# Performance work log

Measured on AMD Instinct MI355X. Metric: run time of the kernel, lower is better.

Reference implementation:

```python
import jax, jax.numpy as jnp
import numpy as np

K = 3  # kernel_size per dim
DIM = 3
NUM_K = K ** DIM  # 27
# the 2^3 corner offsets of the linear B-spline support
OFFS = np.array([[(s >> d) & 1 for d in range(DIM)] for s in range(2 ** DIM)], dtype=np.int32)  # [8,3]
STRIDES = np.array([K ** d for d in range(DIM)], dtype=np.int32)  # [1,3,9]


def bspline_basis(pseudo):
    """Open B-spline basis, degree 1. pseudo: [E,3] in [0,1]. Returns basis [E,8], kidx [E,8]."""
    v = pseudo * (K - 1)
    i0 = jnp.clip(jnp.floor(v), 0, K - 2)
    f = v - i0  # fractional part in [0,1]
    i0 = i0.astype(jnp.int32)
    offs = jnp.asarray(OFFS)  # [8,3]
    w = jnp.where(offs[None].astype(bool), f[:, None, :], 1.0 - f[:, None, :])  # [E,8,3]
    basis = jnp.prod(w, axis=-1)  # [E,8]
    kidx = jnp.sum((i0[:, None, :] + offs[None]) * jnp.asarray(STRIDES)[None, None, :], axis=-1)  # [E,8]
    return basis, kidx


def spline_conv(x, src, dst, pseudo, W, Wroot, b, num_nodes):
    """SplineConv (degree 1, mean aggregation, root weight + bias)."""
    cout = W.shape[-1]
    xW = jnp.einsum('nc,kco->nko', x, W)  # [N,27,Cout]
    basis, kidx = bspline_basis(pseudo)
    flat = src[:, None] * NUM_K + kidx  # [E,8]
    g = xW.reshape(-1, cout)[flat]  # [E,8,Cout] -- dominant gather
    msg = jnp.einsum('es,eso->eo', basis, g)  # [E,Cout]
    agg = jax.ops.segment_sum(msg, dst, num_segments=num_nodes)
    cnt = jax.ops.segment_sum(jnp.ones((src.shape[0],), x.dtype), dst, num_segments=num_nodes)
    return agg / jnp.maximum(cnt, 1.0)[:, None] + x @ Wroot + b


def seg_max(x, seg, num_segments):
    m = jax.ops.segment_max(x, seg, num_segments=num_segments)
    return jnp.where(jnp.isfinite(m), m, 0.0)  # empty clusters -> 0


def setup_inputs() -> dict:
    key = jax.random.key(0)
    ks = jax.random.split(key, 16)
    N, E, B = 80000, 1280000, 16
    N1, N2 = N // 2, N1 if False else (N // 2) // 2  # N1=40000, N2=20000
    N1 = N // 2
    N2 = N1 // 2
    x = jax.random.normal(ks[0], (N, 2), dtype=jnp.float32)
    edge_index = jax.random.randint(ks[1], (2, E), 0, N, dtype=jnp.int32)
    edge_attr = jax.random.uniform(ks[2], (E, 3), dtype=jnp.float32)
    batch = jnp.sort(jax.random.randint(ks[3], (N,), 0, B, dtype=jnp.int32))
    cluster1 = jax.random.randint(ks[4], (N,), 0, N1, dtype=jnp.int32)
    cluster2 = jax.random.randint(ks[5], (N1,), 0, N2, dtype=jnp.int32)
    W1 = jax.random.normal(ks[6], (NUM_K, 2, 8), dtype=jnp.float32) * 0.3
    root1 = jax.random.normal(ks[7], (2, 8), dtype=jnp.float32) * 0.3
    b1 = jnp.zeros((8,), jnp.float32)
    W2 = jax.random.normal(ks[8], (NUM_K, 8, 16), dtype=jnp.float32) * 0.2
    root2 = jax.random.normal(ks[9], (8, 16), dtype=jnp.float32) * 0.2
    b2 = jnp.zeros((16,), jnp.float32)
    fc1_w = jax.random.normal(ks[10], (16, 64), dtype=jnp.float32) * 0.2
    fc1_b = jnp.zeros((64,), jnp.float32)
    fc2_w = jax.random.normal(ks[11], (64, 1), dtype=jnp.float32) * 0.2
    fc2_b = jnp.zeros((1,), jnp.float32)
    return dict(x=x, edge_index=edge_index, edge_attr=edge_attr, batch=batch,
                cluster1=cluster1, cluster2=cluster2,
                W1=W1, root1=root1, b1=b1, W2=W2, root2=root2, b2=b2,
                fc1_w=fc1_w, fc1_b=fc1_b, fc2_w=fc2_w, fc2_b=fc2_b)


def reference(x, edge_index, edge_attr, batch, cluster1, cluster2,
              W1, root1, b1, W2, root2, b2, fc1_w, fc1_b, fc2_w, fc2_b):
    N = x.shape[0]
    N1 = cluster1.max() * 0 + cluster2.shape[0]  # static: 40000
    N1 = cluster2.shape[0]
    N2 = N1 // 2
    B = 16
    src, dst = edge_index[0], edge_index[1]
    # level 1: SplineConv + ELU
    h = jax.nn.elu(spline_conv(x, src, dst, edge_attr, W1, root1, b1, N))
    # max_pool with precomputed cluster assignment (replaces graclus)
    x1 = seg_max(h, cluster1, N1)
    batch1 = jnp.maximum(jax.ops.segment_max(batch, cluster1, num_segments=N1), 0)
    src2 = cluster1[src]
    dst2 = cluster1[dst]
    # level 2: SplineConv + ELU on coarsened graph
    h2 = jax.nn.elu(spline_conv(x1, src2, dst2, edge_attr, W2, root2, b2, N1))
    x2 = seg_max(h2, cluster2, N2)
    batch2 = jnp.maximum(jax.ops.segment_max(batch1, cluster2, num_segments=N2), 0)
    # scatter_mean over graphs
    s = jax.ops.segment_sum(x2, batch2, num_segments=B)
    c = jax.ops.segment_sum(jnp.ones((N2,), x.dtype), batch2, num_segments=B)
    g = s / jnp.maximum(c, 1.0)[:, None]  # [B,16]
    g = jax.nn.elu(g @ fc1_w + fc1_b)  # dropout is identity in eval mode
    return jax.nn.elu(g @ fc2_w + fc2_b)  # [B,1]
```

## Files before the change

kernel.cpp:

```cpp
#include <hip/hip_runtime.h>
#include <hip/hip_fp16.h>
#include <math.h>


__device__ __forceinline__ float eluf(float x) {
    return x > 0.f ? x : (expf(x) - 1.f);
}

__device__ __forceinline__ float hlo(int v) {
    __half2 h; *(int*)&h = v; return __low2float(h);
}
__device__ __forceinline__ float hhi(int v) {
    __half2 h; *(int*)&h = v; return __high2float(h);
}

typedef _Float16 half2v __attribute__((ext_vector_type(2)));

__device__ __forceinline__ half2v uash2(unsigned u) {
    half2v h; *(unsigned*)&h = u; return h;
}

__device__ __forceinline__ float dot2f(half2v a, half2v b, float c) {
#if __has_builtin(__builtin_amdgcn_fdot2)
    return __builtin_amdgcn_fdot2(a, b, c, false);
#else
    return c + (float)a[0] * (float)b[0] + (float)a[1] * (float)b[1];
#endif
}

#define W1_STRIDE 20
#define W2H_STRIDE 68


__global__ __launch_bounds__(256) void hist_kernel(
    const int* __restrict__ ei, const int* __restrict__ cluster1,
    const int* __restrict__ cluster2,
    int* __restrict__ deg, int* __restrict__ rank,
    int* __restrict__ cdeg, int* __restrict__ rankC,
    int* __restrict__ c2deg, int* __restrict__ rank2,
    int E, int N, int N1)
{
    int i = blockIdx.x * 256 + threadIdx.x;
    if (i < E)  rank[i]  = atomicAdd(&deg[ei[E + i]], 1);
    if (i < N)  rankC[i] = atomicAdd(&cdeg[cluster1[i]], 1);
    if (i < N1) rank2[i] = atomicAdd(&c2deg[cluster2[i]], 1);
}

#define SCAN_CHUNK 4096

__global__ __launch_bounds__(256) void scan_a(
    const int* __restrict__ in0, int* __restrict__ out0, int* __restrict__ aux0, int L0, int nb0,
    const int* __restrict__ in1, int* __restrict__ out1, int* __restrict__ aux1, int L1, int nb1,
    const int* __restrict__ in2, int* __restrict__ out2, int* __restrict__ aux2, int L2)
{
    int b = blockIdx.x;
    const int* in; int* out; int* aux; int L;
    if (b < nb0)            { in = in0; out = out0; aux = aux0; L = L0; }
    else if (b < nb0 + nb1) { b -= nb0; in = in1; out = out1; aux = aux1; L = L1; }
    else                    { b -= nb0 + nb1; in = in2; out = out2; aux = aux2; L = L2; }

    __shared__ int ls[256];
    int t = threadIdx.x;
    int base = b * SCAN_CHUNK + t * 16;
    int v[16];
    int s = 0;
#pragma unroll
    for (int j = 0; j < 16; ++j) {
        int val = (base + j < L) ? in[base + j] : 0;
        v[j] = s;
        s += val;
    }
    ls[t] = s;
    __syncthreads();
    for (int off = 1; off < 256; off <<= 1) {
        int tv = (t >= off) ? ls[t - off] : 0;
        __syncthreads();
        ls[t] += tv;
        __syncthreads();
    }
    int excl = ls[t] - s;
#pragma unroll
    for (int j = 0; j < 16; ++j)
        if (base + j < L) out[base + j] = excl + v[j];
    if (t == 255) aux[b] = ls[255];
}

__global__ __launch_bounds__(64) void scan_b(
    int* __restrict__ aux0, int nb0, int* __restrict__ off0, int L0,
    int* __restrict__ aux1, int nb1, int* __restrict__ off1, int L1,
    int* __restrict__ aux2, int nb2, int* __restrict__ off2, int L2)
{
    if (threadIdx.x != 0) return;
    int* aux; int nb; int* off; int L;
    if (blockIdx.x == 0)      { aux = aux0; nb = nb0; off = off0; L = L0; }
    else if (blockIdx.x == 1) { aux = aux1; nb = nb1; off = off1; L = L1; }
    else                      { aux = aux2; nb = nb2; off = off2; L = L2; }
    int run = 0;
    for (int j = 0; j < nb; ++j) { int tv = aux[j]; aux[j] = run; run += tv; }
    off[L] = run;
}

__global__ __launch_bounds__(256) void scan_c(
    int* __restrict__ out0, const int* __restrict__ aux0, int L0, int nb0,
    int* __restrict__ out1, const int* __restrict__ aux1, int L1, int nb1,
    int* __restrict__ out2, const int* __restrict__ aux2, int L2)
{
    int b = blockIdx.x;
    int* out; const int* aux; int L;
    if (b < nb0)            { out = out0; aux = aux0; L = L0; }
    else if (b < nb0 + nb1) { b -= nb0; out = out1; aux = aux1; L = L1; }
    else                    { b -= nb0 + nb1; out = out2; aux = aux2; L = L2; }
    int add = aux[b];
    int base = b * SCAN_CHUNK + threadIdx.x * 16;
#pragma unroll
    for (int j = 0; j < 16; ++j)
        if (base + j < L) out[base + j] += add;
}

__global__ __launch_bounds__(256) void scatB_kernel(
    const int* __restrict__ ei, const float* __restrict__ attr,
    const int* __restrict__ cluster1, const int* __restrict__ cluster2,
    const float2* __restrict__ x, const float* __restrict__ W1,
    const int* __restrict__ doffs, const int* __restrict__ rank,
    const int* __restrict__ coff, const int* __restrict__ rankC,
    const int* __restrict__ c2off, const int* __restrict__ rank2,
    int* __restrict__ nidx, int* __restrict__ n1idx,
    int4* __restrict__ rec4, int E, int N, int N1)
{
    __shared__ float lw[27 * W1_STRIDE];
    for (int i = threadIdx.x; i < 27 * 16; i += 256)
        lw[(i >> 4) * W1_STRIDE + (i & 15)] = W1[i];
    __syncthreads();

    int i = blockIdx.x * 256 + threadIdx.x;
    if (i < E) {
        int s = ei[i], d = ei[E + i];
        int p = doffs[d] + rank[i];

        float vx = attr[3 * i] * 2.f, vy = attr[3 * i + 1] * 2.f, vz = attr[3 * i + 2] * 2.f;
        float ix = fmaxf(fminf(floorf(vx), 1.f), 0.f);
        float iy = fmaxf(fminf(floorf(vy), 1.f), 0.f);
        float iz = fmaxf(fminf(floorf(vz), 1.f), 0.f);
        float fx = vx - ix, fy = vy - iy, fz = vz - iz;
        int ibase = (int)ix + 3 * (int)iy + 9 * (int)iz;

        float2 xv = x[s];
        float wxv[2] = {1.f - fx, fx}, wyv[2] = {1.f - fy, fy}, wzv[2] = {1.f - fz, fz};
        float m[8];
#pragma unroll
        for (int o = 0; o < 8; ++o) m[o] = 0.f;
#pragma unroll
        for (int j = 0; j < 8; ++j) {
            int cx = j & 1, cy = (j >> 1) & 1, cz = j >> 2;
            float w = wxv[cx] * wyv[cy] * wzv[cz];
            const float* Wk = &lw[(ibase + cx + 3 * cy + 9 * cz) * W1_STRIDE];
            float a = w * xv.x, bb = w * xv.y;
            const float4 wa0 = *(const float4*)&Wk[0];
            const float4 wa1 = *(const float4*)&Wk[4];
            const float4 wb0 = *(const float4*)&Wk[8];
            const float4 wb1 = *(const float4*)&Wk[12];
            m[0] += a * wa0.x + bb * wb0.x;
            m[1] += a * wa0.y + bb * wb0.y;
            m[2] += a * wa0.z + bb * wb0.z;
            m[3] += a * wa0.w + bb * wb0.w;
            m[4] += a * wa1.x + bb * wb1.x;
            m[5] += a * wa1.y + bb * wb1.y;
            m[6] += a * wa1.z + bb * wb1.z;
            m[7] += a * wa1.w + bb * wb1.w;
        }

        unsigned hfx = __half_as_ushort(__float2half_rn(fx));
        unsigned hfy = __half_as_ushort(__float2half_rn(fy));
        unsigned hfz = __half_as_ushort(__float2half_rn(fz));
        int s2 = cluster1[s];
        int4 ra = make_int4(s2 | (ibase << 16),
                            (int)(hfx | (hfy << 16)), (int)hfz, 0);
        __half2 h01 = __floats2half2_rn(m[0], m[1]);
        __half2 h23 = __floats2half2_rn(m[2], m[3]);
        __half2 h45 = __floats2half2_rn(m[4], m[5]);
        __half2 h67 = __floats2half2_rn(m[6], m[7]);
        int4 rb = make_int4(*(int*)&h01, *(int*)&h23, *(int*)&h45, *(int*)&h67);
        rec4[2 * (size_t)p]     = ra;
        rec4[2 * (size_t)p + 1] = rb;
    }
    if (i < N)  nidx[coff[cluster1[i]] + rankC[i]] = i;
    if (i < N1) n1idx[c2off[cluster2[i]] + rank2[i]] = i;
}

__global__ __launch_bounds__(256) void reduce1_kernel(
    const int* __restrict__ doffs, const unsigned short* __restrict__ recU,
    float* __restrict__ M1, int N)
{
    int t = blockIdx.x * 256 + threadIdx.x;
    if (t >= N * 8) return;
    int d = t >> 3, ch = t & 7;
    int beg = doffs[d], end = doffs[d + 1];
    float acc = 0.f;
    for (int p = beg; p < end; ++p)
        acc += __half2float(__ushort_as_half(recU[(size_t)p * 16 + 8 + ch]));
    M1[t] = acc / fmaxf((float)(end - beg), 1.f);
}

__global__ __launch_bounds__(256) void node1_kernel(
    const int* __restrict__ coff, const int* __restrict__ nidx,
    const float* __restrict__ M1, const float2* __restrict__ x,
    const float* __restrict__ root1, const float* __restrict__ b1,
    const int* __restrict__ batch,
    float* __restrict__ x1c, unsigned short* __restrict__ x1chU,
    int* __restrict__ batch1, int N1)
{
    int t = blockIdx.x * 256 + threadIdx.x;
    if (t >= N1 * 8) return;
    int c = t >> 3, ch = t & 7;
    int cb = coff[c], ce = coff[c + 1];
    float r0 = root1[ch], r1 = root1[8 + ch], bo = b1[ch];
    float hm = -INFINITY;
    int bm = 0;
    for (int idx = cb; idx < ce; ++idx) {
        int d = nidx[idx];
        float2 xv = x[d];
        float h = eluf(M1[d * 8 + ch] + xv.x * r0 + xv.y * r1 + bo);
        hm = fmaxf(hm, h);
        bm = max(bm, batch[d]);
    }
    if (ce == cb) hm = 0.f;
    x1c[t] = hm;
    x1chU[t] = __half_as_ushort(__float2half_rn(hm));
    if (ch == 0) batch1[c] = bm;
}

__global__ __launch_bounds__(256) void edge2m_kernel(
    const int4* __restrict__ rec4, const unsigned short* __restrict__ x1chU,
    const float* __restrict__ W2, unsigned short* __restrict__ msg2h, int E)
{
    __shared__ unsigned lwh[27 * W2H_STRIDE];
    for (int i = threadIdx.x; i < 27 * 64; i += 256) {
        int k = i >> 6, r = i & 63;
        int o = r >> 2, c2 = r & 3;
        float a = W2[(k * 8 + 2 * c2) * 16 + o];
        float b = W2[(k * 8 + 2 * c2 + 1) * 16 + o];
        __half2 h = __floats2half2_rn(a, b);
        lwh[k * W2H_STRIDE + r] = *(unsigned*)&h;
    }
    __syncthreads();

    int t = blockIdx.x * 256 + threadIdx.x;
    if (t >= E * 4) return;
    int p = t >> 2, oq = t & 3;
    int4 m = rec4[2 * (size_t)p];
    int s2 = m.x & 0xFFFF;
    int ibase = (m.x >> 16) & 31;
    float fx = hlo(m.y), fy = hhi(m.y), fz = hlo(m.z);

    const uint4 xv4 = *(const uint4*)&x1chU[(size_t)s2 * 8];
    half2v xh0 = uash2(xv4.x), xh1 = uash2(xv4.y),
           xh2 = uash2(xv4.z), xh3 = uash2(xv4.w);

    float wx0 = 1.f - fx, wy0 = 1.f - fy, wz0 = 1.f - fz;
    float acc0 = 0.f, acc1 = 0.f, acc2 = 0.f, acc3 = 0.f;
#pragma unroll
    for (int j = 0; j < 8; ++j) {
        int cx = j & 1, cy = (j >> 1) & 1, cz = j >> 2;
        float w = (cx ? fx : wx0) * (cy ? fy : wy0) * (cz ? fz : wz0);
        int k = ibase + cx + 3 * cy + 9 * cz;
        const unsigned* base = &lwh[k * W2H_STRIDE + oq * 16];
        uint4 v0 = *(const uint4*)(base);
        uint4 v1 = *(const uint4*)(base + 4);
        uint4 v2 = *(const uint4*)(base + 8);
        uint4 v3 = *(const uint4*)(base + 12);
        float s0 = dot2f(xh0, uash2(v0.x), dot2f(xh1, uash2(v0.y),
                   dot2f(xh2, uash2(v0.z), dot2f(xh3, uash2(v0.w), 0.f))));
        float s1 = dot2f(xh0, uash2(v1.x), dot2f(xh1, uash2(v1.y),
                   dot2f(xh2, uash2(v1.z), dot2f(xh3, uash2(v1.w), 0.f))));
        float s2v = dot2f(xh0, uash2(v2.x), dot2f(xh1, uash2(v2.y),
                    dot2f(xh2, uash2(v2.z), dot2f(xh3, uash2(v2.w), 0.f))));
        float s3 = dot2f(xh0, uash2(v3.x), dot2f(xh1, uash2(v3.y),
                   dot2f(xh2, uash2(v3.z), dot2f(xh3, uash2(v3.w), 0.f))));
        acc0 = fmaf(w, s0, acc0);
        acc1 = fmaf(w, s1, acc1);
        acc2 = fmaf(w, s2v, acc2);
        acc3 = fmaf(w, s3, acc3);
    }
    __half2 lo = __floats2half2_rn(acc0, acc1);
    __half2 hi = __floats2half2_rn(acc2, acc3);
    uint2 outv = make_uint2(*(unsigned*)&lo, *(unsigned*)&hi);
    *(uint2*)&msg2h[(size_t)p * 16 + oq * 4] = outv;
}

__global__ __launch_bounds__(256) void reduce2_kernel(
    const int* __restrict__ coff, const int* __restrict__ nidx,
    const int* __restrict__ doffs, const unsigned short* __restrict__ msg2h,
    float* __restrict__ M2, int N1)
{
    int t = blockIdx.x * 256 + threadIdx.x;
    if (t >= N1 * 16) return;
    int c = t >> 4, o = t & 15;
    float acc = 0.f;
    int cnt = 0;
    int cb = coff[c], ce = coff[c + 1];
    for (int idx = cb; idx < ce; ++idx) {
        int d = nidx[idx];
        int beg = doffs[d], end = doffs[d + 1];
        cnt += end - beg;
        for (int p = beg; p < end; ++p)
            acc += __half2float(__ushort_as_half(msg2h[(size_t)p * 16 + o]));
    }
    M2[t] = acc / fmaxf((float)cnt, 1.f);
}

__global__ __launch_bounds__(256) void node2_kernel(
    const int* __restrict__ c2off, const int* __restrict__ n1idx,
    const float* __restrict__ M2, const float* __restrict__ x1c,
    const float* __restrict__ root2, const float* __restrict__ b2,
    const int* __restrict__ batch1,
    float* __restrict__ gsum, float* __restrict__ gcnt, int N2)
{
    __shared__ float ls[16 * 16];
    __shared__ float lc[16];
    for (int i = threadIdx.x; i < 256; i += 256) ls[i] = 0.f;
    if (threadIdx.x < 16) lc[threadIdx.x] = 0.f;
    __syncthreads();

    int c2 = blockIdx.x * 256 + threadIdx.x;
    if (c2 < N2) {
        int cb = c2off[c2], ce = c2off[c2 + 1];
        float hm[16];
#pragma unroll
        for (int o = 0; o < 16; ++o) hm[o] = -INFINITY;
        int bm = 0;
        for (int idx = cb; idx < ce; ++idx) {
            int n1 = n1idx[idx];
            const float4* xr4 = (const float4*)&x1c[(size_t)n1 * 8];
            float4 xa = xr4[0], xb = xr4[1];
            float xr[8] = {xa.x, xa.y, xa.z, xa.w, xb.x, xb.y, xb.z, xb.w};
#pragma unroll
            for (int o = 0; o < 16; ++o) {
                float v = M2[(size_t)n1 * 16 + o] + b2[o];
#pragma unroll
                for (int c8 = 0; c8 < 8; ++c8) v += xr[c8] * root2[c8 * 16 + o];
                hm[o] = fmaxf(hm[o], eluf(v));
            }
            bm = max(bm, batch1[n1]);
        }
        if (ce == cb) {
#pragma unroll
            for (int o = 0; o < 16; ++o) hm[o] = 0.f;
        }
#pragma unroll
        for (int o = 0; o < 16; ++o) atomicAdd(&ls[bm * 16 + o], hm[o]);
        atomicAdd(&lc[bm], 1.f);
    }
    __syncthreads();
    for (int i = threadIdx.x; i < 256; i += 256) unsafeAtomicAdd(&gsum[i], ls[i]);
    if (threadIdx.x < 16) unsafeAtomicAdd(&gcnt[threadIdx.x], lc[threadIdx.x]);
}

__global__ __launch_bounds__(256) void head_kernel(
    const float* __restrict__ gsum, const float* __restrict__ gcnt,
    const float* __restrict__ fc1_w, const float* __restrict__ fc1_b,
    const float* __restrict__ fc2_w, const float* __restrict__ fc2_b,
    float* __restrict__ out, int B)
{
    __shared__ float g[16 * 16];
    __shared__ float h1[16 * 64];
    int t = threadIdx.x;
    if (t < B * 16) {
        int b = t >> 4;
        g[t] = gsum[t] / fmaxf(gcnt[b], 1.f);
    }
    __syncthreads();
    for (int j = t; j < B * 64; j += 256) {
        int b = j >> 6, jj = j & 63;
        float s = fc1_b[jj];
#pragma unroll
        for (int c = 0; c < 16; ++c) s += g[b * 16 + c] * fc1_w[c * 64 + jj];
        h1[j] = eluf(s);
    }
    __syncthreads();
    if (t < B) {
        float s = fc2_b[0];
#pragma unroll
        for (int j = 0; j < 64; ++j) s += h1[t * 64 + j] * fc2_w[j];
        out[t] = eluf(s);
    }
}

extern "C" void kernel_launch(void* const* d_in, const int* in_sizes, int n_in,
                              void* d_out, int out_size, void* d_ws, size_t ws_size,
                              hipStream_t stream)
{
    const float* x        = (const float*)d_in[0];
    const int*   ei       = (const int*)  d_in[1];
    const float* attr     = (const float*)d_in[2];
    const int*   batch    = (const int*)  d_in[3];
    const int*   cluster1 = (const int*)  d_in[4];
    const int*   cluster2 = (const int*)  d_in[5];
    const float* W1       = (const float*)d_in[6];
    const float* root1    = (const float*)d_in[7];
    const float* b1       = (const float*)d_in[8];
    const float* W2       = (const float*)d_in[9];
    const float* root2    = (const float*)d_in[10];
    const float* b2       = (const float*)d_in[11];
    const float* fc1_w    = (const float*)d_in[12];
    const float* fc1_b    = (const float*)d_in[13];
    const float* fc2_w    = (const float*)d_in[14];
    const float* fc2_b    = (const float*)d_in[15];

    const int N  = in_sizes[0] / 2;
    const int E  = in_sizes[1] / 2;
    const int N1 = in_sizes[5];
    const int N2 = N1 / 2;
    const int B  = out_size;

    const int nb0 = (N  + SCAN_CHUNK - 1) / SCAN_CHUNK;
    const int nb1 = (N1 + SCAN_CHUNK - 1) / SCAN_CHUNK;
    const int nb2 = (N2 + SCAN_CHUNK - 1) / SCAN_CHUNK;

    int* wi = (int*)d_ws;
    size_t off = 0;
    auto alloc = [&](size_t n, size_t align = 1) {
        off = (off + align - 1) & ~(align - 1);
        size_t r = off; off += n; return r;
    };
    int*   deg    = wi + alloc(N);
    int*   cdeg   = wi + alloc(N1);
    int*   c2deg  = wi + alloc(N2);
    float* gsum   = (float*)(wi + alloc((size_t)B * 16));
    float* gcnt   = (float*)(wi + alloc(B));
    const size_t zcount = off;
    int*   doffs  = wi + alloc(N + 1);
    int*   coff   = wi + alloc(N1 + 1);
    int*   c2off  = wi + alloc(N2 + 1);
    int*   auxA   = wi + alloc(nb0);
    int*   auxB   = wi + alloc(nb1);
    int*   auxC   = wi + alloc(nb2);
    int*   rank   = wi + alloc(E);
    int*   rankC  = wi + alloc(N);
    int*   rank2  = wi + alloc(N1);
    int*   nidx   = wi + alloc(N);
    int*   n1idx  = wi + alloc(N1);
    int4*  rec4   = (int4*)(wi + alloc((size_t)E * 8, 8));
    unsigned short* msg2h = (unsigned short*)(wi + alloc((size_t)E * 8, 4));
    float* M1     = (float*)(wi + alloc((size_t)N * 8, 4));
    float* x1c    = (float*)(wi + alloc((size_t)N1 * 8, 4));
    unsigned short* x1chU = (unsigned short*)(wi + alloc((size_t)N1 * 4, 4));
    int*   batch1 = wi + alloc(N1);
    float* M2     = (float*)(wi + alloc((size_t)N1 * 16, 4));
    (void)ws_size;

    hipMemsetAsync(d_ws, 0, zcount * sizeof(int), stream);

    const int eb = (E + 255) / 256;
    hist_kernel<<<eb, 256, 0, stream>>>(ei, cluster1, cluster2,
                                        deg, rank, cdeg, rankC, c2deg, rank2, E, N, N1);
    scan_a<<<nb0 + nb1 + nb2, 256, 0, stream>>>(deg, doffs, auxA, N, nb0,
                                                cdeg, coff, auxB, N1, nb1,
                                                c2deg, c2off, auxC, N2);
    scan_b<<<3, 64, 0, stream>>>(auxA, nb0, doffs, N,
                                 auxB, nb1, coff, N1,
                                 auxC, nb2, c2off, N2);
    scan_c<<<nb0 + nb1 + nb2, 256, 0, stream>>>(doffs, auxA, N, nb0,
                                                coff, auxB, N1, nb1,
                                                c2off, auxC, N2);
    scatB_kernel<<<eb, 256, 0, stream>>>(ei, attr, cluster1, cluster2,
                                         (const float2*)x, W1,
                                         doffs, rank, coff, rankC, c2off, rank2,
                                         nidx, n1idx, rec4, E, N, N1);
    reduce1_kernel<<<(N * 8 + 255) / 256, 256, 0, stream>>>(
        doffs, (const unsigned short*)rec4, M1, N);
    node1_kernel<<<(N1 * 8 + 255) / 256, 256, 0, stream>>>(
        coff, nidx, M1, (const float2*)x, root1, b1, batch,
        x1c, x1chU, batch1, N1);
    edge2m_kernel<<<(E * 4 + 255) / 256, 256, 0, stream>>>(
        rec4, x1chU, W2, msg2h, E);
    reduce2_kernel<<<(N1 * 16 + 255) / 256, 256, 0, stream>>>(
        coff, nidx, doffs, msg2h, M2, N1);
    node2_kernel<<<(N2 + 255) / 256, 256, 0, stream>>>(
        c2off, n1idx, M2, x1c, root2, b2, batch1, gsum, gcnt, N2);
    head_kernel<<<1, 256, 0, stream>>>(gsum, gcnt, fc1_w, fc1_b, fc2_w, fc2_b,
                                       (float*)d_out, B);
}
```

Baseline: 358.0 us.

## Fuse level-2 edge messages and reduction via per-cluster basis accumulation

Replaces the per-edge message kernel and the separate reduction kernel with a single per-destination-cluster kernel. Each cluster first accumulates basis-weighted input features into a 27x8 shared-memory tile, then applies W2 once per kernel slot, which avoids writing and re-reading a per-edge fp16 message buffer and cuts the weight multiplies. The cost is a large shared-memory footprint (about 28KB per block), which limits occupancy. Load balance also depends on how many edges each cluster owns, and the half-precision conversion now happens on accumulated sums.

```diff
diff --git a/kernel.cpp b/kernel.cpp
--- a/kernel.cpp
+++ b/kernel.cpp
@@ -18,6 +18,11 @@
 
 __device__ __forceinline__ half2v uash2(unsigned u) {
     half2v h; *(unsigned*)&h = u; return h;
+}
+
+__device__ __forceinline__ half2v f2h2(float a, float b) {
+    __half2 h = __floats2half2_rn(a, b);
+    return *(half2v*)&h;
 }
 
 __device__ __forceinline__ float dot2f(half2v a, half2v b, float c) {
@@ -206,8 +211,7 @@
     const float* __restrict__ M1, const float2* __restrict__ x,
     const float* __restrict__ root1, const float* __restrict__ b1,
     const int* __restrict__ batch,
-    float* __restrict__ x1c, unsigned short* __restrict__ x1chU,
-    int* __restrict__ batch1, int N1)
+    float* __restrict__ x1c, int* __restrict__ batch1, int N1)
 {
     int t = blockIdx.x * 256 + threadIdx.x;
     if (t >= N1 * 8) return;
@@ -225,15 +229,19 @@
     }
     if (ce == cb) hm = 0.f;
     x1c[t] = hm;
-    x1chU[t] = __half_as_ushort(__float2half_rn(hm));
     if (ch == 0) batch1[c] = bm;
 }
 
-__global__ __launch_bounds__(256) void edge2m_kernel(
-    const int4* __restrict__ rec4, const unsigned short* __restrict__ x1chU,
-    const float* __restrict__ W2, unsigned short* __restrict__ msg2h, int E)
-{
+__global__ __launch_bounds__(256) void edge2f_kernel(
+    const int* __restrict__ coff, const int* __restrict__ nidx,
+    const int* __restrict__ doffs, const int4* __restrict__ rec4,
+    const float* __restrict__ x1c, const float* __restrict__ W2,
+    float* __restrict__ M2, int N1)
+{
+    __shared__ float A[27 * 32 * 8];
     __shared__ unsigned lwh[27 * W2H_STRIDE];
+    __shared__ float lcnt[32];
+
     for (int i = threadIdx.x; i < 27 * 64; i += 256) {
         int k = i >> 6, r = i & 63;
         int o = r >> 2, c2 = r & 3;
@@ -242,70 +250,66 @@
         __half2 h = __floats2half2_rn(a, b);
         lwh[k * W2H_STRIDE + r] = *(unsigned*)&h;
     }
-    __syncthreads();
-
-    int t = blockIdx.x * 256 + threadIdx.x;
-    if (t >= E * 4) return;
-    int p = t >> 2, oq = t & 3;
-    int4 m = rec4[2 * (size_t)p];
-    int s2 = m.x & 0xFFFF;
-    int ibase = (m.x >> 16) & 31;
-    float fx = hlo(m.y), fy = hhi(m.y), fz = hlo(m.z);
-
-    const uint4 xv4 = *(const uint4*)&x1chU[(size_t)s2 * 8];
-    half2v xh0 = uash2(xv4.x), xh1 = uash2(xv4.y),
-           xh2 = uash2(xv4.z), xh3 = uash2(xv4.w);
-
-    float wx0 = 1.f - fx, wy0 = 1.f - fy, wz0 = 1.f - fz;
-    float acc0 = 0.f, acc1 = 0.f, acc2 = 0.f, acc3 = 0.f;
-#pragma unroll
-    for (int j = 0; j < 8; ++j) {
-        int cx = j & 1, cy = (j >> 1) & 1, cz = j >> 2;
-        float w = (cx ? fx : wx0) * (cy ? fy : wy0) * (cz ? fz : wz0);
-        int k = ibase + cx + 3 * cy + 9 * cz;
-        const unsigned* base = &lwh[k * W2H_STRIDE + oq * 16];
-        uint4 v0 = *(const uint4*)(base);
-        uint4 v1 = *(const uint4*)(base + 4);
-        uint4 v2 = *(const uint4*)(base + 8);
-        uint4 v3 = *(const uint4*)(base + 12);
-        float s0 = dot2f(xh0, uash2(v0.x), dot2f(xh1, uash2(v0.y),
-                   dot2f(xh2, uash2(v0.z), dot2f(xh3, uash2(v0.w), 0.f))));
-        float s1 = dot2f(xh0, uash2(v1.x), dot2f(xh1, uash2(v1.y),
-                   dot2f(xh2, uash2(v1.z), dot2f(xh3, uash2(v1.w), 0.f))));
-        float s2v = dot2f(xh0, uash2(v2.x), dot2f(xh1, uash2(v2.y),
-                    dot2f(xh2, uash2(v2.z), dot2f(xh3, uash2(v2.w), 0.f))));
-        float s3 = dot2f(xh0, uash2(v3.x), dot2f(xh1, uash2(v3.y),
-                   dot2f(xh2, uash2(v3.z), dot2f(xh3, uash2(v3.w), 0.f))));
-        acc0 = fmaf(w, s0, acc0);
-        acc1 = fmaf(w, s1, acc1);
-        acc2 = fmaf(w, s2v, acc2);
-        acc3 = fmaf(w, s3, acc3);
-    }
-    __half2 lo = __floats2half2_rn(acc0, acc1);
-    __half2 hi = __floats2half2_rn(acc2, acc3);
-    uint2 outv = make_uint2(*(unsigned*)&lo, *(unsigned*)&hi);
-    *(uint2*)&msg2h[(size_t)p * 16 + oq * 4] = outv;
-}
-
-__global__ __launch_bounds__(256) void reduce2_kernel(
-    const int* __restrict__ coff, const int* __restrict__ nidx,
-    const int* __restrict__ doffs, const unsigned short* __restrict__ msg2h,
-    float* __restrict__ M2, int N1)
-{
-    int t = blockIdx.x * 256 + threadIdx.x;
-    if (t >= N1 * 16) return;
-    int c = t >> 4, o = t & 15;
-    float acc = 0.f;
-    int cnt = 0;
-    int cb = coff[c], ce = coff[c + 1];
-    for (int idx = cb; idx < ce; ++idx) {
-        int d = nidx[idx];
-        int beg = doffs[d], end = doffs[d + 1];
-        cnt += end - beg;
-        for (int p = beg; p < end; ++p)
-            acc += __half2float(__ushort_as_half(msg2h[(size_t)p * 16 + o]));
-    }
-    M2[t] = acc / fmaxf((float)cnt, 1.f);
+    for (int i = threadIdx.x; i < 27 * 32 * 8; i += 256) A[i] = 0.f;
+    if (threadIdx.x < 32) lcnt[threadIdx.x] = 0.f;
+    __syncthreads();
+
+    int cl = threadIdx.x >> 3, ch = threadIdx.x & 7;
+    int c = blockIdx.x * 32 + cl;
+    if (c < N1) {
+        int cnt = 0;
+        int cb = coff[c], ce = coff[c + 1];
+        for (int idx = cb; idx < ce; ++idx) {
+            int d = nidx[idx];
+            int beg = doffs[d], end = doffs[d + 1];
+            cnt += end - beg;
+            for (int p = beg; p < end; ++p) {
+                int4 m = rec4[2 * (size_t)p];
+                int s2 = m.x & 0xFFFF;
+                int ibase = (m.x >> 16) & 31;
+                float fx = hlo(m.y), fy = hhi(m.y), fz = hlo(m.z);
+                float xv = x1c[s2 * 8 + ch];
+                float wx0 = 1.f - fx, wy0 = 1.f - fy, wz0 = 1.f - fz;
+                float w00 = wy0 * wz0, w10 = fy * wz0;
+                float w01 = wy0 * fz,  w11 = fy * fz;
+                int base = ibase * 256 + cl * 8 + ch;
+                A[base]            += (wx0 * w00) * xv;
+                A[base + 1 * 256]  += (fx  * w00) * xv;
+                A[base + 3 * 256]  += (wx0 * w10) * xv;
+                A[base + 4 * 256]  += (fx  * w10) * xv;
+                A[base + 9 * 256]  += (wx0 * w01) * xv;
+                A[base + 10 * 256] += (fx  * w01) * xv;
+                A[base + 12 * 256] += (wx0 * w11) * xv;
+                A[base + 13 * 256] += (fx  * w11) * xv;
+            }
+        }
+        if (ch == 0) lcnt[cl] = (float)cnt;
+    }
+    __syncthreads();
+
+    if (c < N1) {
+        int o2 = ch;
+        float acc0 = 0.f, acc1 = 0.f;
+        for (int k = 0; k < 27; ++k) {
+            const float4* ar = (const float4*)&A[k * 256 + cl * 8];
+            float4 a0 = ar[0], a1 = ar[1];
+            half2v pa0 = f2h2(a0.x, a0.y), pa1 = f2h2(a0.z, a0.w);
+            half2v pa2 = f2h2(a1.x, a1.y), pa3 = f2h2(a1.z, a1.w);
+            const uint4 w0 = *(const uint4*)&lwh[k * W2H_STRIDE + o2 * 4];
+            const uint4 w1 = *(const uint4*)&lwh[k * W2H_STRIDE + (o2 + 8) * 4];
+            acc0 = dot2f(pa0, uash2(w0.x), acc0);
+            acc0 = dot2f(pa1, uash2(w0.y), acc0);
+            acc0 = dot2f(pa2, uash2(w0.z), acc0);
+            acc0 = dot2f(pa3, uash2(w0.w), acc0);
+            acc1 = dot2f(pa0, uash2(w1.x), acc1);
+            acc1 = dot2f(pa1, uash2(w1.y), acc1);
+            acc1 = dot2f(pa2, uash2(w1.z), acc1);
+            acc1 = dot2f(pa3, uash2(w1.w), acc1);
+        }
+        float inv = 1.f / fmaxf(lcnt[cl], 1.f);
+        M2[(size_t)c * 16 + o2]     = acc0 * inv;
+        M2[(size_t)c * 16 + o2 + 8] = acc1 * inv;
+    }
 }
 
 __global__ __launch_bounds__(256) void node2_kernel(
@@ -440,10 +444,8 @@
     int*   nidx   = wi + alloc(N);
     int*   n1idx  = wi + alloc(N1);
     int4*  rec4   = (int4*)(wi + alloc((size_t)E * 8, 8));
-    unsigned short* msg2h = (unsigned short*)(wi + alloc((size_t)E * 8, 4));
     float* M1     = (float*)(wi + alloc((size_t)N * 8, 4));
     float* x1c    = (float*)(wi + alloc((size_t)N1 * 8, 4));
-    unsigned short* x1chU = (unsigned short*)(wi + alloc((size_t)N1 * 4, 4));
     int*   batch1 = wi + alloc(N1);
     float* M2     = (float*)(wi + alloc((size_t)N1 * 16, 4));
     (void)ws_size;
@@ -470,11 +472,9 @@
         doffs, (const unsigned short*)rec4, M1, N);
     node1_kernel<<<(N1 * 8 + 255) / 256, 256, 0, stream>>>(
         coff, nidx, M1, (const float2*)x, root1, b1, batch,
-        x1c, x1chU, batch1, N1);
-    edge2m_kernel<<<(E * 4 + 255) / 256, 256, 0, stream>>>(
-        rec4, x1chU, W2, msg2h, E);
-    reduce2_kernel<<<(N1 * 16 + 255) / 256, 256, 0, stream>>>(
-        coff, nidx, doffs, msg2h, M2, N1);
+        x1c, batch1, N1);
+    edge2f_kernel<<<(N1 + 31) / 32, 256, 0, stream>>>(
+        coff, nidx, doffs, rec4, x1c, W2, M2, N1);
     node2_kernel<<<(N2 + 255) / 256, 256, 0, stream>>>(
         c2off, n1idx, M2, x1c, root2, b2, batch1, gsum, gcnt, N2);
     head_kernel<<<1, 256, 0, stream>>>(gsum, gcnt, fc1_w, fc1_b, fc2_w, fc2_b,
```

Measured after the change: 379.4 us. +6.0%, slower.
